# Optimization experiments

Hardware: AMD Instinct MI355X
Metric: run time of the kernel (lower is better)

Reference implementation:

```python
import jax, jax.numpy as jnp
import numpy as np

DIM = 1024
HEADS = 16
HEAD_DIM = DIM // HEADS
SCALE = HEAD_DIM ** -0.5


def setup_inputs() -> dict:
    key = jax.random.key(0)
    k_x, k_qkv, k_ow, k_ob = jax.random.split(key, 4)
    B, N = 4, 2048
    x = jax.random.normal(k_x, (B, N, DIM), dtype=jnp.float32)
    # nn.Linear(dim, 3*dim, bias=False): weight [3*dim, dim]; we store transposed [dim, 3*dim]
    w_qkv = jax.random.normal(k_qkv, (DIM, 3 * DIM), dtype=jnp.float32) * (DIM ** -0.5)
    w_out = jax.random.normal(k_ow, (DIM, DIM), dtype=jnp.float32) * (DIM ** -0.5)
    b_out = jax.random.normal(k_ob, (DIM,), dtype=jnp.float32) * 0.01
    return {"x": x, "w_qkv": w_qkv, "w_out": w_out, "b_out": b_out}


def reference(x, w_qkv, w_out, b_out):
    B, N, D = x.shape
    H, hd = HEADS, HEAD_DIM
    qkv = x @ w_qkv                                  # [B, N, 3D]
    qkv = qkv.reshape(B, N, 3, H, hd).transpose(2, 0, 3, 1, 4)  # [3, B, H, N, hd]
    q, k, v = qkv[0], qkv[1], qkv[2]
    dots = jnp.einsum('bhnd,bhmd->bhnm', q, k) * SCALE  # [B, H, N, N]
    attn = jax.nn.softmax(dots, axis=-1)
    out = jnp.einsum('bhnm,bhmd->bhnd', attn, v)     # [B, H, N, hd]
    out = out.transpose(0, 2, 1, 3).reshape(B, N, D)
    return out @ w_out + b_out
```

## Files before the change

### kernel.cpp

```cpp
#include <hip/hip_runtime.h>
#include <hip/hip_bf16.h>

#define BSZ   4
#define NSEQ  2048
#define DIMM  1024
#define NHEAD 16
#define HD    64
#define N3    (3*DIMM)
#define MTOK  (BSZ*NSEQ)
#define SCALE 0.125f
#define CQ    0.18033688011112042f

typedef __attribute__((ext_vector_type(8))) short    short8;
typedef __attribute__((ext_vector_type(4))) short    short4v;
typedef __attribute__((ext_vector_type(2))) unsigned uint2v;
typedef __attribute__((ext_vector_type(8))) __bf16   bf16x8;
typedef __attribute__((ext_vector_type(4))) float    f32x4;

__device__ inline short f2bf(float f) {
    unsigned u = __builtin_bit_cast(unsigned, f);
    u += 0x7fffu + ((u >> 16) & 1u);
    return (short)(u >> 16);
}

__device__ inline unsigned pack_bf16(float a, float b) {
    unsigned ua = __builtin_bit_cast(unsigned, a) + 0x8000u;
    unsigned ub = __builtin_bit_cast(unsigned, b) + 0x8000u;
    return __builtin_amdgcn_perm(ub, ua, 0x07060302u);
}

__device__ inline float fast_exp2(float x) {
#if __has_builtin(__builtin_amdgcn_exp2f)
    return __builtin_amdgcn_exp2f(x);
#else
    return exp2f(x);
#endif
}

__device__ inline bf16x8 lds_frag(const short* p) {
    return __builtin_bit_cast(bf16x8, *(const short8*)p);
}

__device__ inline bf16x8 glb_frag(const short* p) {
    return __builtin_bit_cast(bf16x8, *(const short8*)p);
}

__device__ inline void gld_lds16(const short* g, short* l) {
    __builtin_amdgcn_global_load_lds(
        (const __attribute__((address_space(1))) void*)g,
        (__attribute__((address_space(3))) void*)l, 16, 0, 0);
}

__global__ __launch_bounds__(256)
void cvt_bf16(const float* __restrict__ src, short* __restrict__ dst, int n8)
{
    int i = blockIdx.x * 256 + threadIdx.x;
    if (i >= n8) return;
    float4 v0 = ((const float4*)src)[i * 2];
    float4 v1 = ((const float4*)src)[i * 2 + 1];
    short8 s = { f2bf(v0.x), f2bf(v0.y), f2bf(v0.z), f2bf(v0.w),
                 f2bf(v1.x), f2bf(v1.y), f2bf(v1.z), f2bf(v1.w) };
    ((short8*)dst)[i] = s;
}

__global__ __launch_bounds__(256)
void transpose_bf16(const float* __restrict__ src, short* __restrict__ dst,
                    int K, int N)
{
    __shared__ float tile[32][33];
    const int n0 = blockIdx.x * 32, k0 = blockIdx.y * 32;
    const int tx = threadIdx.x, ty = threadIdx.y;
    #pragma unroll
    for (int i = 0; i < 4; ++i)
        tile[ty + i * 8][tx] = src[(size_t)(k0 + ty + i * 8) * N + n0 + tx];
    __syncthreads();
    #pragma unroll
    for (int i = 0; i < 4; ++i)
        dst[(size_t)(n0 + ty + i * 8) * K + k0 + tx] = f2bf(tile[tx][ty + i * 8]);
}

#define GEMM_KLOOP(APTR, BPTR)                                                 \
    for (int k0 = 0; k0 < DIMM; k0 += 32) {                                    \
        _Pragma("unroll")                                                      \
        for (int j = 0; j < 2; ++j) {                                          \
            int c = j * 256 + tid;                                             \
            int r = c >> 2, jj = c & 3;                                        \
            int gc = jj ^ ((r >> 1) & 3);                                      \
            gld_lds16(APTR + (size_t)(row0 + r) * DIMM + k0 + gc * 8,          \
                      As + c * 8);                                             \
            gld_lds16(BPTR + (size_t)(col0 + r) * DIMM + k0 + gc * 8,         \
                      Bs + c * 8);                                             \
        }                                                                      \
        __syncthreads();                                                       \
        bf16x8 af[4], bfr[4];                                                  \
        _Pragma("unroll")                                                      \
        for (int mt = 0; mt < 4; ++mt) {                                       \
            int row = wm + mt * 16 + l16;                                      \
            af[mt] = lds_frag(&As[row * 32 + (quad ^ ((row >> 1) & 3)) * 8]);  \
        }                                                                      \
        _Pragma("unroll")                                                      \
        for (int nt = 0; nt < 4; ++nt) {                                       \
            int row = wn + nt * 16 + l16;                                      \
            bfr[nt] = lds_frag(&Bs[row * 32 + (quad ^ ((row >> 1) & 3)) * 8]); \
        }                                                                      \
        _Pragma("unroll")                                                      \
        for (int mt = 0; mt < 4; ++mt)                                         \
            _Pragma("unroll")                                                  \
            for (int nt = 0; nt < 4; ++nt)                                     \
                acc[mt][nt] = __builtin_amdgcn_mfma_f32_16x16x32_bf16(         \
                    af[mt], bfr[nt], acc[mt][nt], 0, 0, 0);                    \
        __syncthreads();                                                       \
    }

__global__ __launch_bounds__(256, 2)
void gemm_qkv(const short* __restrict__ a, const short* __restrict__ bt,
              short* __restrict__ qo, short* __restrict__ ko,
              short* __restrict__ vo)
{
    __shared__ short As[128 * 32];
    __shared__ short Bs[128 * 32];
    const int tid  = threadIdx.x;
    const int wave = tid >> 6, lane = tid & 63;
    const int quad = lane >> 4, l16 = lane & 15;
    const int row0 = blockIdx.x * 128, col0 = blockIdx.y * 128;
    const int wm = (wave >> 1) * 64, wn = (wave & 1) * 64;

    f32x4 acc[4][4] = {};
    GEMM_KLOOP(a, bt)

    #pragma unroll
    for (int mt = 0; mt < 4; ++mt) {
        #pragma unroll
        for (int nt = 0; nt < 4; ++nt) {
            int gcol  = col0 + wn + nt * 16 + l16;
            int which = gcol >> 10;
            int cc    = gcol & 1023;
            int h     = cc >> 6, d = cc & 63;
            int growb = row0 + wm + mt * 16 + quad * 4;
            int b_    = growb >> 11;
            int n_    = growb & 2047;
            int bh    = b_ * NHEAD + h;
            if (which == 2) {
                short4v s = { f2bf(acc[mt][nt][0]), f2bf(acc[mt][nt][1]),
                              f2bf(acc[mt][nt][2]), f2bf(acc[mt][nt][3]) };
                *(short4v*)(vo + ((size_t)bh * HD + d) * NSEQ + n_) = s;
            } else if (which == 0) {
                #pragma unroll
                for (int r = 0; r < 4; ++r)
                    qo[((size_t)bh * NSEQ + n_ + r) * HD + d] =
                        f2bf(acc[mt][nt][r] * CQ);
            } else {
                #pragma unroll
                for (int r = 0; r < 4; ++r)
                    ko[((size_t)bh * NSEQ + n_ + r) * HD + d] = f2bf(acc[mt][nt][r]);
            }
        }
    }
}

__global__ __launch_bounds__(256, 3)
void attn(const short* __restrict__ q, const short* __restrict__ k,
          const short* __restrict__ vt, short* __restrict__ o)
{
    __shared__ short Ks[2][64 * 64];
    __shared__ short Ps[4][32 * 72];

    const int tid  = threadIdx.x;
    const int wave = tid >> 6, lane = tid & 63;
    const int quad = lane >> 4, l16 = lane & 15;
    const int bh   = blockIdx.y;
    const int q0   = blockIdx.x * 128;
    const size_t qkbase = (size_t)bh * NSEQ * HD;
    const size_t vbase  = (size_t)bh * HD * NSEQ;

    bf16x8 qf[2][2];
    #pragma unroll
    for (int g = 0; g < 2; ++g)
        #pragma unroll
        for (int ks = 0; ks < 2; ++ks)
            qf[g][ks] = glb_frag(q + qkbase +
                (size_t)(q0 + wave * 32 + g * 16 + l16) * HD + ks * 32 + quad * 8);

    f32x4 oacc[4][2] = {};
    float lsum[2] = {0.f, 0.f};
    short* Pw = &Ps[wave][0];

    const int  sr   = tid >> 3, sj = tid & 7;
    const int  soff = sr * HD + ((sj ^ (sr & 7)) * 8);
    const short* kbh = k + qkbase;

    gld_lds16(kbh + soff,            &Ks[0][tid * 8]);
    gld_lds16(kbh + soff + 32 * HD,  &Ks[0][2048 + tid * 8]);

    for (int t = 0; t < NSEQ / 64; ++t) {
        const int kv0 = t * 64;
        __syncthreads();
        if (t + 1 < NSEQ / 64) {
            const short* src = kbh + (size_t)(kv0 + 64) * HD;
            short* dst = &Ks[(t + 1) & 1][0];
            gld_lds16(src + soff,           dst + tid * 8);
            gld_lds16(src + soff + 32 * HD, dst + 2048 + tid * 8);
        }
        const short* Kb = &Ks[t & 1][0];

        bf16x8 vf[2][4];
        #pragma unroll
        for (int ks2 = 0; ks2 < 2; ++ks2)
            #pragma unroll
            for (int ot = 0; ot < 4; ++ot)
                vf[ks2][ot] = glb_frag(vt + vbase +
                    (size_t)(ot * 16 + l16) * NSEQ + kv0 + ks2 * 32 + quad * 8);

        f32x4 sacc[4][2] = {};
        #pragma unroll
        for (int nt = 0; nt < 4; ++nt) {
            int row = nt * 16 + l16;
            #pragma unroll
            for (int ks = 0; ks < 2; ++ks) {
                bf16x8 kf = lds_frag(&Kb[row * 64 + (((ks * 4 + quad) ^ (row & 7)) * 8)]);
                #pragma unroll
                for (int g = 0; g < 2; ++g)
                    sacc[nt][g] = __builtin_amdgcn_mfma_f32_16x16x32_bf16(
                        kf, qf[g][ks], sacc[nt][g], 0, 0, 0);
            }
        }

        #pragma unroll
        for (int g = 0; g < 2; ++g) {
            #pragma unroll
            for (int nt = 0; nt < 4; ++nt) {
                float p0 = fast_exp2(sacc[nt][g][0]);
                float p1 = fast_exp2(sacc[nt][g][1]);
                float p2 = fast_exp2(sacc[nt][g][2]);
                float p3 = fast_exp2(sacc[nt][g][3]);
                lsum[g] += (p0 + p1) + (p2 + p3);
                uint2v u = { pack_bf16(p0, p1), pack_bf16(p2, p3) };
                *(uint2v*)&Pw[(g * 16 + l16) * 72 + nt * 16 + quad * 4] = u;
            }
        }

        #pragma unroll
        for (int ks2 = 0; ks2 < 2; ++ks2) {
            bf16x8 pf[2];
            #pragma unroll
            for (int g = 0; g < 2; ++g)
                pf[g] = lds_frag(&Pw[(g * 16 + l16) * 72 + ks2 * 32 + quad * 8]);
            #pragma unroll
            for (int ot = 0; ot < 4; ++ot)
                #pragma unroll
                for (int g = 0; g < 2; ++g)
                    oacc[ot][g] = __builtin_amdgcn_mfma_f32_16x16x32_bf16(
                        vf[ks2][ot], pf[g], oacc[ot][g], 0, 0, 0);
        }
    }

    const int b_ = bh >> 4, h = bh & 15;
    float inv[2];
    #pragma unroll
    for (int g = 0; g < 2; ++g) {
        float l = lsum[g];
        l += __shfl_xor(l, 16);
        l += __shfl_xor(l, 32);
        inv[g] = 1.f / l;
    }
    #pragma unroll
    for (int ot = 0; ot < 4; ++ot) {
        #pragma unroll
        for (int g = 0; g < 2; ++g) {
            short4v s4 = { f2bf(oacc[ot][g][0] * inv[g]),
                           f2bf(oacc[ot][g][1] * inv[g]),
                           f2bf(oacc[ot][g][2] * inv[g]),
                           f2bf(oacc[ot][g][3] * inv[g]) };
            *(short4v*)(o + ((size_t)b_ * NSEQ + q0 + wave * 32 + g * 16 + l16) * DIMM +
                        h * HD + ot * 16 + quad * 4) = s4;
        }
    }
}

__global__ __launch_bounds__(256, 2)
void gemm_out(const short* __restrict__ a, const short* __restrict__ bt,
              const float* __restrict__ bias, float* __restrict__ out)
{
    __shared__ short As[128 * 32];
    __shared__ short Bs[128 * 32];
    const int tid  = threadIdx.x;
    const int wave = tid >> 6, lane = tid & 63;
    const int quad = lane >> 4, l16 = lane & 15;
    const int row0 = blockIdx.x * 128, col0 = blockIdx.y * 128;
    const int wm = (wave >> 1) * 64, wn = (wave & 1) * 64;

    f32x4 acc[4][4] = {};
    GEMM_KLOOP(a, bt)

    #pragma unroll
    for (int mt = 0; mt < 4; ++mt) {
        #pragma unroll
        for (int nt = 0; nt < 4; ++nt) {
            int gcol = col0 + wn + nt * 16 + l16;
            float bb = bias[gcol];
            #pragma unroll
            for (int r = 0; r < 4; ++r) {
                int grow = row0 + wm + mt * 16 + quad * 4 + r;
                out[(size_t)grow * DIMM + gcol] = acc[mt][nt][r] + bb;
            }
        }
    }
}

extern "C" void kernel_launch(void* const* d_in, const int* in_sizes, int n_in,
                              void* d_out, int out_size, void* d_ws, size_t ws_size,
                              hipStream_t stream)
{
    const float* x     = (const float*)d_in[0];
    const float* w_qkv = (const float*)d_in[1];
    const float* w_out = (const float*)d_in[2];
    const float* b_out = (const float*)d_in[3];
    float* out = (float*)d_out;

    const size_t per = (size_t)BSZ * NHEAD * NSEQ * HD;
    short* q     = (short*)d_ws;
    short* kk    = q  + per;
    short* v     = kk + per;
    short* xb_ob = v  + per;
    short* wqkvT = xb_ob + per;
    short* woutT = wqkvT + (size_t)N3 * DIMM;

    cvt_bf16<<<(int)(per / 8 / 256), 256, 0, stream>>>(x, xb_ob, (int)(per / 8));
    transpose_bf16<<<dim3(N3 / 32, DIMM / 32), dim3(32, 8), 0, stream>>>(w_qkv, wqkvT, DIMM, N3);
    transpose_bf16<<<dim3(DIMM / 32, DIMM / 32), dim3(32, 8), 0, stream>>>(w_out, woutT, DIMM, DIMM);

    gemm_qkv<<<dim3(MTOK / 128, N3 / 128), 256, 0, stream>>>(xb_ob, wqkvT, q, kk, v);
    attn<<<dim3(NSEQ / 128, BSZ * NHEAD), 256, 0, stream>>>(q, kk, v, xb_ob);
    gemm_out<<<dim3(MTOK / 128, DIMM / 128), 256, 0, stream>>>(xb_ob, woutT, b_out, out);
}
```

Measured before the change: 315.4 us.

## Load K fragments directly from global memory instead of LDS double buffer

Removes the shared-memory double-buffered K tile and its per-iteration __syncthreads. Each wave now loads K MFMA fragments straight from global memory in two halves, and launch bounds go from 3 to 4 blocks per CU. This drops the block barrier and frees LDS, but every wave now fetches the full K tile from global/L2 on its own, which quadruples K read traffic per block and exposes load latency without an explicit prefetch.

```diff
diff --git a/kernel.cpp b/kernel.cpp
--- a/kernel.cpp
+++ b/kernel.cpp
@@ -158,11 +158,10 @@
     }
 }
 
-__global__ __launch_bounds__(256, 3)
+__global__ __launch_bounds__(256, 4)
 void attn(const short* __restrict__ q, const short* __restrict__ k,
           const short* __restrict__ vt, short* __restrict__ o)
 {
-    __shared__ short Ks[2][64 * 64];
     __shared__ short Ps[4][32 * 72];
 
     const int tid  = threadIdx.x;
@@ -184,24 +183,33 @@
     f32x4 oacc[4][2] = {};
     float lsum[2] = {0.f, 0.f};
     short* Pw = &Ps[wave][0];
-
-    const int  sr   = tid >> 3, sj = tid & 7;
-    const int  soff = sr * HD + ((sj ^ (sr & 7)) * 8);
     const short* kbh = k + qkbase;
-
-    gld_lds16(kbh + soff,            &Ks[0][tid * 8]);
-    gld_lds16(kbh + soff + 32 * HD,  &Ks[0][2048 + tid * 8]);
 
     for (int t = 0; t < NSEQ / 64; ++t) {
         const int kv0 = t * 64;
-        __syncthreads();
-        if (t + 1 < NSEQ / 64) {
-            const short* src = kbh + (size_t)(kv0 + 64) * HD;
-            short* dst = &Ks[(t + 1) & 1][0];
-            gld_lds16(src + soff,           dst + tid * 8);
-            gld_lds16(src + soff + 32 * HD, dst + 2048 + tid * 8);
-        }
-        const short* Kb = &Ks[t & 1][0];
+        f32x4 sacc[4][2] = {};
+
+        #pragma unroll
+        for (int half = 0; half < 2; ++half) {
+            bf16x8 kf[2][2];
+            #pragma unroll
+            for (int nt2 = 0; nt2 < 2; ++nt2)
+                #pragma unroll
+                for (int ks = 0; ks < 2; ++ks)
+                    kf[nt2][ks] = glb_frag(kbh +
+                        (size_t)(kv0 + (half * 2 + nt2) * 16 + l16) * HD +
+                        ks * 32 + quad * 8);
+            #pragma unroll
+            for (int nt2 = 0; nt2 < 2; ++nt2)
+                #pragma unroll
+                for (int ks = 0; ks < 2; ++ks)
+                    #pragma unroll
+                    for (int g = 0; g < 2; ++g)
+                        sacc[half * 2 + nt2][g] =
+                            __builtin_amdgcn_mfma_f32_16x16x32_bf16(
+                                kf[nt2][ks], qf[g][ks], sacc[half * 2 + nt2][g],
+                                0, 0, 0);
+        }
 
         bf16x8 vf[2][4];
         #pragma unroll
@@ -210,20 +218,6 @@
             for (int ot = 0; ot < 4; ++ot)
                 vf[ks2][ot] = glb_frag(vt + vbase +
                     (size_t)(ot * 16 + l16) * NSEQ + kv0 + ks2 * 32 + quad * 8);
-
-        f32x4 sacc[4][2] = {};
-        #pragma unroll
-        for (int nt = 0; nt < 4; ++nt) {
-            int row = nt * 16 + l16;
-            #pragma unroll
-            for (int ks = 0; ks < 2; ++ks) {
-                bf16x8 kf = lds_frag(&Kb[row * 64 + (((ks * 4 + quad) ^ (row & 7)) * 8)]);
-                #pragma unroll
-                for (int g = 0; g < 2; ++g)
-                    sacc[nt][g] = __builtin_amdgcn_mfma_f32_16x16x32_bf16(
-                        kf, qf[g][ks], sacc[nt][g], 0, 0, 0);
-            }
-        }
 
         #pragma unroll
         for (int g = 0; g < 2; ++g) {
```

New measurement: 414.8 us. 31.5% more time.

## Software-pipeline attention loop: overlap softmax of tile t-1 with QK of tile t

Applied to the files above, without the earlier changes.

Restructures the attention inner loop so the exp/softmax and PV product for the previous KV tile are interleaved with the QK^T MFMA for the current tile, with a prologue and epilogue. The aim is to let VALU exp work and MFMA work from different tiles overlap instead of running back to back. It also adds s_setprio around the MFMA blocks to favour matrix issue. The cost is more live registers (sacc is held across iterations) under launch_bounds(256,3), which may cause spills or lower occupancy.

```diff
diff --git a/kernel.cpp b/kernel.cpp
--- a/kernel.cpp
+++ b/kernel.cpp
@@ -158,6 +158,67 @@
     }
 }
 
+#define S_PHASE(KBUF)                                                          \
+    { _Pragma("unroll")                                                        \
+      for (int nt = 0; nt < 4; ++nt)                                           \
+          _Pragma("unroll")                                                    \
+          for (int g = 0; g < 2; ++g)                                          \
+              sacc[nt][g] = (f32x4){0.f, 0.f, 0.f, 0.f};                       \
+      __builtin_amdgcn_s_setprio(1);                                           \
+      _Pragma("unroll")                                                        \
+      for (int nt = 0; nt < 4; ++nt) {                                         \
+          int row = nt * 16 + l16;                                             \
+          _Pragma("unroll")                                                    \
+          for (int ks = 0; ks < 2; ++ks) {                                     \
+              bf16x8 kf = lds_frag(&(KBUF)[row * 64 +                          \
+                              (((ks * 4 + quad) ^ (row & 7)) * 8)]);           \
+              _Pragma("unroll")                                                \
+              for (int g = 0; g < 2; ++g)                                      \
+                  sacc[nt][g] = __builtin_amdgcn_mfma_f32_16x16x32_bf16(       \
+                      kf, qf[g][ks], sacc[nt][g], 0, 0, 0);                    \
+          }                                                                    \
+      }                                                                        \
+      __builtin_amdgcn_s_setprio(0); }
+
+#define SM_PHASE                                                               \
+    { _Pragma("unroll")                                                        \
+      for (int g = 0; g < 2; ++g)                                              \
+          _Pragma("unroll")                                                    \
+          for (int nt = 0; nt < 4; ++nt) {                                     \
+              float p0 = fast_exp2(sacc[nt][g][0]);                            \
+              float p1 = fast_exp2(sacc[nt][g][1]);                            \
+              float p2 = fast_exp2(sacc[nt][g][2]);                            \
+              float p3 = fast_exp2(sacc[nt][g][3]);                            \
+              lsum[g] += (p0 + p1) + (p2 + p3);                                \
+              uint2v u = { pack_bf16(p0, p1), pack_bf16(p2, p3) };             \
+              *(uint2v*)&Pw[(g * 16 + l16) * 72 + nt * 16 + quad * 4] = u;     \
+          } }
+
+#define VF_LOAD(KV0)                                                           \
+    _Pragma("unroll")                                                          \
+    for (int ks2 = 0; ks2 < 2; ++ks2)                                          \
+        _Pragma("unroll")                                                      \
+        for (int ot = 0; ot < 4; ++ot)                                         \
+            vf[ks2][ot] = glb_frag(vt + vbase +                                \
+                (size_t)(ot * 16 + l16) * NSEQ + (KV0) + ks2 * 32 + quad * 8);
+
+#define PV_PHASE                                                               \
+    _Pragma("unroll")                                                          \
+    for (int ks2 = 0; ks2 < 2; ++ks2) {                                        \
+        bf16x8 pf[2];                                                          \
+        _Pragma("unroll")                                                      \
+        for (int g = 0; g < 2; ++g)                                            \
+            pf[g] = lds_frag(&Pw[(g * 16 + l16) * 72 + ks2 * 32 + quad * 8]);  \
+        __builtin_amdgcn_s_setprio(1);                                         \
+        _Pragma("unroll")                                                      \
+        for (int ot = 0; ot < 4; ++ot)                                         \
+            _Pragma("unroll")                                                  \
+            for (int g = 0; g < 2; ++g)                                        \
+                oacc[ot][g] = __builtin_amdgcn_mfma_f32_16x16x32_bf16(         \
+                    vf[ks2][ot], pf[g], oacc[ot][g], 0, 0, 0);                 \
+        __builtin_amdgcn_s_setprio(0);                                         \
+    }
+
 __global__ __launch_bounds__(256, 3)
 void attn(const short* __restrict__ q, const short* __restrict__ k,
           const short* __restrict__ vt, short* __restrict__ o)
@@ -189,69 +250,34 @@
     const int  soff = sr * HD + ((sj ^ (sr & 7)) * 8);
     const short* kbh = k + qkbase;
 
-    gld_lds16(kbh + soff,            &Ks[0][tid * 8]);
-    gld_lds16(kbh + soff + 32 * HD,  &Ks[0][2048 + tid * 8]);
-
-    for (int t = 0; t < NSEQ / 64; ++t) {
-        const int kv0 = t * 64;
+    gld_lds16(kbh + soff,           &Ks[0][tid * 8]);
+    gld_lds16(kbh + soff + 32 * HD, &Ks[0][2048 + tid * 8]);
+    __syncthreads();
+    gld_lds16(kbh + 64 * HD + soff,           &Ks[1][tid * 8]);
+    gld_lds16(kbh + 64 * HD + soff + 32 * HD, &Ks[1][2048 + tid * 8]);
+
+    f32x4 sacc[4][2];
+    S_PHASE(&Ks[0][0])
+
+    for (int t = 1; t < NSEQ / 64; ++t) {
+        const int kvp = (t - 1) * 64;
+        SM_PHASE
         __syncthreads();
+        bf16x8 vf[2][4];
+        VF_LOAD(kvp)
         if (t + 1 < NSEQ / 64) {
-            const short* src = kbh + (size_t)(kv0 + 64) * HD;
-            short* dst = &Ks[(t + 1) & 1][0];
-            gld_lds16(src + soff,           dst + tid * 8);
-            gld_lds16(src + soff + 32 * HD, dst + 2048 + tid * 8);
+            const short* src = kbh + (size_t)(t + 1) * 64 * HD;
+            gld_lds16(src + soff,           &Ks[(t + 1) & 1][tid * 8]);
+            gld_lds16(src + soff + 32 * HD, &Ks[(t + 1) & 1][2048 + tid * 8]);
         }
-        const short* Kb = &Ks[t & 1][0];
-
+        S_PHASE(&Ks[t & 1][0])
+        PV_PHASE
+    }
+    {
+        SM_PHASE
         bf16x8 vf[2][4];
-        #pragma unroll
-        for (int ks2 = 0; ks2 < 2; ++ks2)
-            #pragma unroll
-            for (int ot = 0; ot < 4; ++ot)
-                vf[ks2][ot] = glb_frag(vt + vbase +
-                    (size_t)(ot * 16 + l16) * NSEQ + kv0 + ks2 * 32 + quad * 8);
-
-        f32x4 sacc[4][2] = {};
-        #pragma unroll
-        for (int nt = 0; nt < 4; ++nt) {
-            int row = nt * 16 + l16;
-            #pragma unroll
-            for (int ks = 0; ks < 2; ++ks) {
-                bf16x8 kf = lds_frag(&Kb[row * 64 + (((ks * 4 + quad) ^ (row & 7)) * 8)]);
-                #pragma unroll
-                for (int g = 0; g < 2; ++g)
-                    sacc[nt][g] = __builtin_amdgcn_mfma_f32_16x16x32_bf16(
-                        kf, qf[g][ks], sacc[nt][g], 0, 0, 0);
-            }
-        }
-
-        #pragma unroll
-        for (int g = 0; g < 2; ++g) {
-            #pragma unroll
-            for (int nt = 0; nt < 4; ++nt) {
-                float p0 = fast_exp2(sacc[nt][g][0]);
-                float p1 = fast_exp2(sacc[nt][g][1]);
-                float p2 = fast_exp2(sacc[nt][g][2]);
-                float p3 = fast_exp2(sacc[nt][g][3]);
-                lsum[g] += (p0 + p1) + (p2 + p3);
-                uint2v u = { pack_bf16(p0, p1), pack_bf16(p2, p3) };
-                *(uint2v*)&Pw[(g * 16 + l16) * 72 + nt * 16 + quad * 4] = u;
-            }
-        }
-
-        #pragma unroll
-        for (int ks2 = 0; ks2 < 2; ++ks2) {
-            bf16x8 pf[2];
-            #pragma unroll
-            for (int g = 0; g < 2; ++g)
-                pf[g] = lds_frag(&Pw[(g * 16 + l16) * 72 + ks2 * 32 + quad * 8]);
-            #pragma unroll
-            for (int ot = 0; ot < 4; ++ot)
-                #pragma unroll
-                for (int g = 0; g < 2; ++g)
-                    oacc[ot][g] = __builtin_amdgcn_mfma_f32_16x16x32_bf16(
-                        vf[ks2][ot], pf[g], oacc[ot][g], 0, 0, 0);
-        }
+        VF_LOAD(NSEQ - 64)
+        PV_PHASE
     }
 
     const int b_ = bh >> 4, h = bh & 15;
```

After: 341.5 us. 1.08x slower.

## Rearrange attention P fragments in registers with permlane swaps instead of LDS

Applied to the files above, without the earlier changes.

Replaces the per-wave LDS round trip for the softmax probability tile (write P to shared memory, read back as MFMA B-operand fragments) with in-register permlane32/permlane16 swaps that rebuild the required bf16x8 layout. This removes the P shared buffer and its LDS traffic and waits, and raises launch bounds from 3 to 4 blocks per CU now that LDS usage is smaller. The risks are register pressure under the tighter occupancy bound and the correctness of the cross-lane permutation mapping.

```diff
diff --git a/kernel.cpp b/kernel.cpp
--- a/kernel.cpp
+++ b/kernel.cpp
@@ -13,7 +13,7 @@
 
 typedef __attribute__((ext_vector_type(8))) short    short8;
 typedef __attribute__((ext_vector_type(4))) short    short4v;
-typedef __attribute__((ext_vector_type(2))) unsigned uint2v;
+typedef __attribute__((ext_vector_type(4))) unsigned uint4v;
 typedef __attribute__((ext_vector_type(8))) __bf16   bf16x8;
 typedef __attribute__((ext_vector_type(4))) float    f32x4;
 
@@ -35,6 +35,13 @@
 #else
     return exp2f(x);
 #endif
+}
+
+__device__ inline void pl32swap(unsigned& a, unsigned& b) {
+    asm("v_permlane32_swap_b32 %0, %1" : "+v"(a), "+v"(b));
+}
+__device__ inline void pl16swap(unsigned& a, unsigned& b) {
+    asm("v_permlane16_swap_b32 %0, %1" : "+v"(a), "+v"(b));
 }
 
 __device__ inline bf16x8 lds_frag(const short* p) {
@@ -158,12 +165,11 @@
     }
 }
 
-__global__ __launch_bounds__(256, 3)
+__global__ __launch_bounds__(256, 4)
 void attn(const short* __restrict__ q, const short* __restrict__ k,
           const short* __restrict__ vt, short* __restrict__ o)
 {
     __shared__ short Ks[2][64 * 64];
-    __shared__ short Ps[4][32 * 72];
 
     const int tid  = threadIdx.x;
     const int wave = tid >> 6, lane = tid & 63;
@@ -183,7 +189,6 @@
 
     f32x4 oacc[4][2] = {};
     float lsum[2] = {0.f, 0.f};
-    short* Pw = &Ps[wave][0];
 
     const int  sr   = tid >> 3, sj = tid & 7;
     const int  soff = sr * HD + ((sj ^ (sr & 7)) * 8);
@@ -225,33 +230,39 @@
             }
         }
 
+        bf16x8 pw[2][2];
         #pragma unroll
         for (int g = 0; g < 2; ++g) {
+            float p[4][4];
             #pragma unroll
             for (int nt = 0; nt < 4; ++nt) {
-                float p0 = fast_exp2(sacc[nt][g][0]);
-                float p1 = fast_exp2(sacc[nt][g][1]);
-                float p2 = fast_exp2(sacc[nt][g][2]);
-                float p3 = fast_exp2(sacc[nt][g][3]);
-                lsum[g] += (p0 + p1) + (p2 + p3);
-                uint2v u = { pack_bf16(p0, p1), pack_bf16(p2, p3) };
-                *(uint2v*)&Pw[(g * 16 + l16) * 72 + nt * 16 + quad * 4] = u;
-            }
-        }
-
-        #pragma unroll
-        for (int ks2 = 0; ks2 < 2; ++ks2) {
-            bf16x8 pf[2];
-            #pragma unroll
-            for (int g = 0; g < 2; ++g)
-                pf[g] = lds_frag(&Pw[(g * 16 + l16) * 72 + ks2 * 32 + quad * 8]);
+                p[nt][0] = fast_exp2(sacc[nt][g][0]);
+                p[nt][1] = fast_exp2(sacc[nt][g][1]);
+                p[nt][2] = fast_exp2(sacc[nt][g][2]);
+                p[nt][3] = fast_exp2(sacc[nt][g][3]);
+                lsum[g] += (p[nt][0] + p[nt][1]) + (p[nt][2] + p[nt][3]);
+            }
+            #pragma unroll
+            for (int ks2 = 0; ks2 < 2; ++ks2) {
+                unsigned A0 = pack_bf16(p[2 * ks2][0],     p[2 * ks2][1]);
+                unsigned B0 = pack_bf16(p[2 * ks2][2],     p[2 * ks2][3]);
+                unsigned A1 = pack_bf16(p[2 * ks2 + 1][0], p[2 * ks2 + 1][1]);
+                unsigned B1 = pack_bf16(p[2 * ks2 + 1][2], p[2 * ks2 + 1][3]);
+                pl32swap(A0, A1); pl16swap(A0, A1);
+                pl32swap(B0, B1); pl16swap(B0, B1);
+                uint4v w = { A0, B0, A1, B1 };
+                pw[g][ks2] = __builtin_bit_cast(bf16x8, w);
+            }
+        }
+
+        #pragma unroll
+        for (int ks2 = 0; ks2 < 2; ++ks2)
             #pragma unroll
             for (int ot = 0; ot < 4; ++ot)
                 #pragma unroll
                 for (int g = 0; g < 2; ++g)
                     oacc[ot][g] = __builtin_amdgcn_mfma_f32_16x16x32_bf16(
-                        vf[ks2][ot], pf[g], oacc[ot][g], 0, 0, 0);
-        }
+                        vf[ks2][ot], pw[g][ks2], oacc[ot][g], 0, 0, 0);
     }
 
     const int b_ = bh >> 4, h = bh & 15;
```

Result: no change. 316.2 us (+0.3%).
